# Kernel tuning notes

Hardware: AMD Instinct MI355X
Metric: run time of the kernel (lower is better)

The kernel has to match this reference:

```python
import jax, jax.numpy as jnp
import numpy as np

B, T, I, H, NM = 128, 512, 2, 1024, 8
MS = H // NM  # module size = 128


def setup_inputs() -> dict:
    key = jax.random.key(0)
    ks = jax.random.split(key, 6)
    s = 1.0 / np.sqrt(H)
    return {
        "x": jax.random.normal(ks[0], (B, T + 1, I, 1), jnp.float32),
        "W_ih": jax.random.normal(ks[1], (H, I), jnp.float32) * s,
        "W_hh": jax.random.normal(ks[2], (H, H), jnp.float32) * s,
        "fc_w": jax.random.normal(ks[3], (I, H), jnp.float32) * s,
        "fc_b": jax.random.normal(ks[4], (I,), jnp.float32) * s,
        "enc_w": jax.random.normal(ks[5], (H, I), jnp.float32) * s,
    }


def reference(x, W_ih, W_hh, fc_w, fc_b, enc_w):
    # x: [B, T+1, I, 1] -> squeeze trailing dim
    xs = x[..., 0]                       # [B, T+1, I]
    h0 = xs[:, 0] @ enc_w.T              # start_encoder (no bias) -> [B, H]

    # Clockwork block structure: row-module i reads hidden cols >= i*MS.
    mod_idx = jnp.arange(H) // MS
    mask_hh = (mod_idx[None, :] >= mod_idx[:, None]).astype(W_hh.dtype)
    Whh_m = W_hh * mask_hh               # block upper-triangular recurrent weights
    periods = 2 ** jnp.arange(NM)        # module clock periods [1,2,4,...,128]

    def step(h, inp):
        x_t, t = inp                     # x_t: [B, I], t: scalar step index
        cand = jnp.tanh(x_t @ W_ih.T + h @ Whh_m.T)          # [B, H]
        active = jnp.repeat((t % periods) == 0, MS)          # [H] unit-level clock mask
        h_new = jnp.where(active[None, :], cand, h)          # inactive modules keep state
        return h_new, h_new @ fc_w.T + fc_b                  # fc output per step

    _, outs = jax.lax.scan(step, h0, (jnp.swapaxes(xs[:, 1:], 0, 1), jnp.arange(T)))
    return jnp.swapaxes(outs, 0, 1)      # [B, T, I]
```

## Files before the change

kernel.cpp:

```cpp
#include <hip/hip_runtime.h>
#include <hip/hip_fp16.h>
#include <math.h>

#define Bsz 128
#define Tsz 512
#define Hsz 1024
#define MS  128
#define NT  512


__global__ __launch_bounds__(256)
void retile_whh(const float* __restrict__ W, __half* __restrict__ WBr) {
    const int p = blockIdx.x + 1;
    const int t = threadIdx.x;
    int c = 0;
    while ((c+1)*(c+2)/2 <= p) ++c;
    const int r = p - c*(c+1)/2;
    __half* wb = WBr + (size_t)(p-1) * MS * MS;
    for (int idx = t; idx < MS*MS; idx += 256) {
        const int row = idx >> 7, j = idx & (MS-1);
        wb[idx] = __float2half(W[(size_t)(r*MS+row)*Hsz + c*MS + j]);
    }
}

__device__ __forceinline__ float fast_tanh(float x) {
    const float e = __expf(2.0f * x);
    return 1.0f - 2.0f * __builtin_amdgcn_rcpf(e + 1.0f);
}

template <int CTRL>
__device__ __forceinline__ float dpp_get(float v) {
    union { float f; int i; } u, o;
    u.f = v;
    o.i = __builtin_amdgcn_update_dpp(0, u.i, CTRL, 0xf, 0xf, true);
    return o.f;
}

__device__ __forceinline__ void pk_fma(float2& acc, float2 a, float2 b) {
    asm("v_pk_fma_f32 %0, %1, %2, %0" : "+v"(acc) : "v"(a), "v"(b));
}

union H4 { short4 s4; __half2 h2[2]; };
union F4 { float4 v; float2 h[2]; };

__global__ __launch_bounds__(NT)
void cwrnn_kernel(const float* __restrict__ x,
                  const float* __restrict__ W_ih,
                  const float* __restrict__ fc_w,
                  const float* __restrict__ fc_b,
                  const float* __restrict__ enc_w,
                  const float* __restrict__ Whh,
                  const __half* __restrict__ WBr,
                  float* __restrict__ out)
{
    __shared__ float   Sp2s[36][MS];
    __shared__ float   h_s[Hsz];
    __shared__ float   H0[2][MS];
    __shared__ float2  x_s[Tsz+1];
    __shared__ float2  wih_s[Hsz];
    __shared__ float2  fcw_s[Hsz];
    __shared__ float2  OpM0[2][8];
    __shared__ float2  OpHi[16];
    __shared__ float2  OpHiN[16];

    const int tid   = threadIdx.x;
    const int lane  = tid & 63;
    const int wave  = tid >> 6;
    const int b     = blockIdx.x;
    const int row00 = tid >> 2;
    const int jc    = tid & 3;

    const float2* xb = (const float2*)(x + (size_t)b*(Tsz+1)*2);
    float* outb = out + (size_t)b*Tsz*2;

    for (int i = tid; i < Tsz+1; i += NT) x_s[i] = xb[i];
    for (int i = tid; i < Hsz; i += NT) wih_s[i] = ((const float2*)W_ih)[i];
    for (int i = tid; i < Hsz; i += NT) fcw_s[i] = make_float2(fc_w[i], fc_w[Hsz+i]);
    if (tid < 16) { OpHi[tid] = make_float2(0.f,0.f); OpHiN[tid] = make_float2(0.f,0.f); }
    const float fb0 = fc_b[0], fb1 = fc_b[1];

    F4 w00[8], w01[8], w11[8];
    #pragma unroll
    for (int u = 0; u < 8; ++u) {
        const int uu = (u + 2*jc) & 7;
        const int j  = jc*32 + uu*4;
        w00[u].v = *(const float4*)(Whh + (size_t)row00*Hsz + j);
        w01[u].v = *(const float4*)(Whh + (size_t)row00*Hsz + MS + j);
        w11[u].v = *(const float4*)(Whh + (size_t)(MS + row00)*Hsz + MS + j);
    }
    short4 w02[8];
    #pragma unroll
    for (int u = 0; u < 8; ++u) {
        const int uu = (u + 2*jc) & 7;
        w02[u] = *(const short4*)(WBr + (size_t)2*MS*MS + row00*MS + jc*32 + uu*4);
    }

    {
        const float2 x0 = xb[0];
        for (int i = tid; i < Hsz; i += NT) {
            const float2 ew = ((const float2*)enc_w)[i];
            const float v = x0.x*ew.x + x0.y*ew.y;
            h_s[i] = v;
            if (i < MS) H0[0][i] = v;
        }
    }
    __syncthreads();

    float R1=0.f,R2=0.f,R3=0.f,R4=0.f,R5=0.f,R6=0.f,R7=0.f;

    auto load_hq = [&](int c, F4* hq) {
        #pragma unroll
        for (int u = 0; u < 8; ++u) {
            const int uu = (u + 2*jc) & 7;
            hq[u].v = *(const float4*)(h_s + c*MS + jc*32 + uu*4);
        }
    };
    auto pair_acc32 = [&](const F4* w, const F4* hq) -> float {
        float2 a0 = {0.f,0.f}, a1 = {0.f,0.f};
        #pragma unroll
        for (int u = 0; u < 8; ++u) {
            pk_fma(a0, w[u].h[0], hq[u].h[0]);
            pk_fma(a1, w[u].h[1], hq[u].h[1]);
        }
        return (a0.x + a0.y) + (a1.x + a1.y);
    };
    auto pair_acc16 = [&](const short4* w, const F4* hq) -> float {
        float2 a0 = {0.f,0.f}, a1 = {0.f,0.f};
        #pragma unroll
        for (int u = 0; u < 8; ++u) {
            H4 ww; ww.s4 = w[u];
            pk_fma(a0, __half22float2(ww.h2[0]), hq[u].h[0]);
            pk_fma(a1, __half22float2(ww.h2[1]), hq[u].h[1]);
        }
        return (a0.x + a0.y) + (a1.x + a1.y);
    };
    auto wg_load = [&](int p, short4* w) {
        const __half* base = WBr + (size_t)(p-1)*MS*MS + row00*MS;
        #pragma unroll
        for (int u = 0; u < 8; ++u) {
            const int uu = (u + 2*jc) & 7;
            w[u] = *(const short4*)(base + jc*32 + uu*4);
        }
    };

    auto do_cols = [&](int ashad) {
        F4 hq[8];
        short4 wA[8], wB[8];
        if (ashad >= 2) wg_load(4, wA);
        load_hq(1, hq);
        R1 = pair_acc32(w01, hq);
        { float aa = pair_acc32(w11, hq);
          aa += dpp_get<0xB1>(aa); aa += dpp_get<0x4E>(aa);
          if (jc == 0) Sp2s[2][row00] = aa; }
        if (ashad >= 2) {
            load_hq(2, hq);
            R2 = pair_acc16(w02, hq);
            int cc = 2, rr = 1;
            while (true) {
                int rn = rr + 1, cn = cc;
                if (rn > cn) { cn += 1; rn = 0; }
                const bool hn = (cn <= ashad);
                if (hn) wg_load(cn*(cn+1)/2 + rn, wB);
                float aa = pair_acc16(wA, hq);
                if (rr == 0) {
                    switch (cc) {
                        case 3: R3 = aa; break;
                        case 4: R4 = aa; break;
                        case 5: R5 = aa; break;
                        case 6: R6 = aa; break;
                        default: R7 = aa; break;
                    }
                } else {
                    aa += dpp_get<0xB1>(aa); aa += dpp_get<0x4E>(aa);
                    if (jc == 0) Sp2s[cc*(cc+1)/2 + rr][row00] = aa;
                }
                if (!hn) break;
                if (cn != cc) load_hq(cn, hq);
                cc = cn; rr = rn;
                #pragma unroll
                for (int u = 0; u < 8; ++u) wA[u] = wB[u];
            }
        }
    };

    do_cols(7);
    __syncthreads();

    for (int t = 0; t < Tsz; ++t) {
        const int A  = (t == 0) ? 7 : ((t & 1) ? 0 : min(__ffs(t)-1, 7));
        const int ap = (t & 1) ? ((t == 1) ? 7 : min(__ffs(t-1)-1, 7)) : 0;
        const float2 xt = x_s[t+1];

        if (ap >= 1) do_cols(ap);

        {
            const float* h0r = H0[t & 1];
            float2 a0 = {0.f,0.f}, a1 = {0.f,0.f};
            #pragma unroll
            for (int u = 0; u < 8; ++u) {
                const int uu = (u + 2*jc) & 7;
                F4 hv; hv.v = *(const float4*)(h0r + jc*32 + uu*4);
                pk_fma(a0, w00[u].h[0], hv.h[0]);
                pk_fma(a1, w00[u].h[1], hv.h[1]);
            }
            float a = (a0.x + a0.y) + (a1.x + a1.y);
            a += ((R1+R2)+(R3+R4)) + ((R5+R6)+R7);
            a += dpp_get<0xB1>(a); a += dpp_get<0x4E>(a);
            const float2 wih0 = wih_s[row00];
            const float hv0 = fast_tanh(a + xt.x*wih0.x + xt.y*wih0.y);
            if (jc == 0) H0[(t+1)&1][row00] = hv0;
            const float2 fw0 = fcw_s[row00];
            float o0 = (jc == 0) ? hv0*fw0.x : 0.f;
            float o1 = (jc == 0) ? hv0*fw0.y : 0.f;
            o0 += dpp_get<0x111>(o0); o1 += dpp_get<0x111>(o1);
            o0 += dpp_get<0x112>(o0); o1 += dpp_get<0x112>(o1);
            o0 += dpp_get<0x114>(o0); o1 += dpp_get<0x114>(o1);
            o0 += dpp_get<0x118>(o0); o1 += dpp_get<0x118>(o1);
            o0 += dpp_get<0x142>(o0); o1 += dpp_get<0x142>(o1);
            o0 += dpp_get<0x143>(o0); o1 += dpp_get<0x143>(o1);
            if (lane == 63) OpM0[t&1][wave] = make_float2(o0, o1);
        }

        if (A >= 1) {
            const int nrows = (A+1)*MS;
            {
                const int g = MS + tid;
                if (g < nrows) {
                    const int r = g >> 7, il = g & (MS-1);
                    float sc[8];
                    #pragma unroll
                    for (int c = 1; c < 8; ++c)
                        sc[c] = Sp2s[c*(c+1)/2 + ((c < r) ? c : r)][il];
                    const float2 wih2 = wih_s[g];
                    float pre = xt.x*wih2.x + xt.y*wih2.y;
                    #pragma unroll
                    for (int c = 1; c < 8; ++c) pre += (c >= r) ? sc[c] : 0.f;
                    const float hv = fast_tanh(pre);
                    h_s[g] = hv;
                    const float2 fw = fcw_s[g];
                    float o0 = hv*fw.x, o1 = hv*fw.y;
                    o0 += dpp_get<0x111>(o0); o1 += dpp_get<0x111>(o1);
                    o0 += dpp_get<0x112>(o0); o1 += dpp_get<0x112>(o1);
                    o0 += dpp_get<0x114>(o0); o1 += dpp_get<0x114>(o1);
                    o0 += dpp_get<0x118>(o0); o1 += dpp_get<0x118>(o1);
                    o0 += dpp_get<0x142>(o0); o1 += dpp_get<0x142>(o1);
                    o0 += dpp_get<0x143>(o0); o1 += dpp_get<0x143>(o1);
                    if (lane == 63) OpHiN[2 + wave] = make_float2(o0, o1);
                }
            }
            {
                const int g = 5*MS + tid;
                if (g < nrows) {
                    const int r = g >> 7, il = g & (MS-1);
                    float sc[8];
                    #pragma unroll
                    for (int c = 1; c < 8; ++c)
                        sc[c] = Sp2s[c*(c+1)/2 + ((c < r) ? c : r)][il];
                    const float2 wih2 = wih_s[g];
                    float pre = xt.x*wih2.x + xt.y*wih2.y;
                    #pragma unroll
                    for (int c = 1; c < 8; ++c) pre += (c >= r) ? sc[c] : 0.f;
                    const float hv = fast_tanh(pre);
                    h_s[g] = hv;
                    const float2 fw = fcw_s[g];
                    float o0 = hv*fw.x, o1 = hv*fw.y;
                    o0 += dpp_get<0x111>(o0); o1 += dpp_get<0x111>(o1);
                    o0 += dpp_get<0x112>(o0); o1 += dpp_get<0x112>(o1);
                    o0 += dpp_get<0x114>(o0); o1 += dpp_get<0x114>(o1);
                    o0 += dpp_get<0x118>(o0); o1 += dpp_get<0x118>(o1);
                    o0 += dpp_get<0x142>(o0); o1 += dpp_get<0x142>(o1);
                    o0 += dpp_get<0x143>(o0); o1 += dpp_get<0x143>(o1);
                    if (lane == 63) OpHiN[10 + wave] = make_float2(o0, o1);
                }
            }
        }

        if (t > 0 && tid == 0) {
            const int tp = t - 1;
            if (ap >= 1) {
                for (int k = 2; k <= 2*ap+1; ++k) OpHi[k] = OpHiN[k];
            }
            float o0 = fb0, o1 = fb1;
            #pragma unroll
            for (int w = 0; w < 8; ++w) { o0 += OpM0[tp&1][w].x; o1 += OpM0[tp&1][w].y; }
            #pragma unroll
            for (int k = 2; k < 16; ++k) { o0 += OpHi[k].x; o1 += OpHi[k].y; }
            *(float2*)(outb + 2*tp) = make_float2(o0, o1);
        }

        __syncthreads();
    }

    if (tid == 0) {
        float o0 = fb0, o1 = fb1;
        #pragma unroll
        for (int w = 0; w < 8; ++w) { o0 += OpM0[1][w].x; o1 += OpM0[1][w].y; }
        #pragma unroll
        for (int k = 2; k < 16; ++k) { o0 += OpHi[k].x; o1 += OpHi[k].y; }
        *(float2*)(outb + 2*(Tsz-1)) = make_float2(o0, o1);
    }
}

extern "C" void kernel_launch(void* const* d_in, const int* in_sizes, int n_in,
                              void* d_out, int out_size, void* d_ws, size_t ws_size,
                              hipStream_t stream) {
    const float* x     = (const float*)d_in[0];
    const float* W_ih  = (const float*)d_in[1];
    const float* W_hh  = (const float*)d_in[2];
    const float* fc_w  = (const float*)d_in[3];
    const float* fc_b  = (const float*)d_in[4];
    const float* enc_w = (const float*)d_in[5];
    float* outp = (float*)d_out;
    __half* WBr = (__half*)((char*)d_ws + 65536);

    retile_whh<<<35, 256, 0, stream>>>(W_hh, WBr);
    cwrnn_kernel<<<Bsz, NT, 0, stream>>>(x, W_ih, fc_w, fc_b, enc_w, W_hh, WBr, outp);
}
```

Before: 1.087 ms.

## Hold more fp16 recurrent blocks in registers and prefetch module-0 hidden state

Converts the register-resident W01 and W11 blocks from fp32 to fp16 and adds W12 and W22 as register-resident fp16 blocks. The streamed-weight loop therefore starts at column 3 instead of column 2. Weight loads become 16-byte int4 loads without the per-thread rotation, and the module-0 hidden vector is loaded before do_cols so its latency overlaps that work. Adds launch_bounds minimum blocks of 2, which constrains registers and risks spills. Removing the rotation may also raise LDS bank conflicts, and fp16 for W01/W11 lowers precision.

```diff
diff --git a/kernel.cpp b/kernel.cpp
--- a/kernel.cpp
+++ b/kernel.cpp
@@ -43,7 +43,7 @@
 union H4 { short4 s4; __half2 h2[2]; };
 union F4 { float4 v; float2 h[2]; };
 
-__global__ __launch_bounds__(NT)
+__global__ __launch_bounds__(NT, 2)
 void cwrnn_kernel(const float* __restrict__ x,
                   const float* __restrict__ W_ih,
                   const float* __restrict__ fc_w,
@@ -79,20 +79,22 @@
     if (tid < 16) { OpHi[tid] = make_float2(0.f,0.f); OpHiN[tid] = make_float2(0.f,0.f); }
     const float fb0 = fc_b[0], fb1 = fc_b[1];
 
-    F4 w00[8], w01[8], w11[8];
+    F4 w00[8];
     #pragma unroll
-    for (int u = 0; u < 8; ++u) {
-        const int uu = (u + 2*jc) & 7;
-        const int j  = jc*32 + uu*4;
-        w00[u].v = *(const float4*)(Whh + (size_t)row00*Hsz + j);
-        w01[u].v = *(const float4*)(Whh + (size_t)row00*Hsz + MS + j);
-        w11[u].v = *(const float4*)(Whh + (size_t)(MS + row00)*Hsz + MS + j);
-    }
-    short4 w02[8];
-    #pragma unroll
-    for (int u = 0; u < 8; ++u) {
-        const int uu = (u + 2*jc) & 7;
-        w02[u] = *(const short4*)(WBr + (size_t)2*MS*MS + row00*MS + jc*32 + uu*4);
+    for (int u = 0; u < 8; ++u)
+        w00[u].v = *(const float4*)(Whh + (size_t)row00*Hsz + jc*32 + u*4);
+
+    short4 w01[8], w02[8], w11[8], w12[8], w22[8];
+    {
+        const __half* base = WBr + row00*MS + jc*32;
+        #pragma unroll
+        for (int u = 0; u < 4; ++u) {
+            *(int4*)(&w01[2*u]) = *(const int4*)(base + (size_t)0*MS*MS + u*8);
+            *(int4*)(&w11[2*u]) = *(const int4*)(base + (size_t)1*MS*MS + u*8);
+            *(int4*)(&w02[2*u]) = *(const int4*)(base + (size_t)2*MS*MS + u*8);
+            *(int4*)(&w12[2*u]) = *(const int4*)(base + (size_t)3*MS*MS + u*8);
+            *(int4*)(&w22[2*u]) = *(const int4*)(base + (size_t)4*MS*MS + u*8);
+        }
     }
 
     {
@@ -110,19 +112,8 @@
 
     auto load_hq = [&](int c, F4* hq) {
         #pragma unroll
-        for (int u = 0; u < 8; ++u) {
-            const int uu = (u + 2*jc) & 7;
-            hq[u].v = *(const float4*)(h_s + c*MS + jc*32 + uu*4);
-        }
-    };
-    auto pair_acc32 = [&](const F4* w, const F4* hq) -> float {
-        float2 a0 = {0.f,0.f}, a1 = {0.f,0.f};
-        #pragma unroll
-        for (int u = 0; u < 8; ++u) {
-            pk_fma(a0, w[u].h[0], hq[u].h[0]);
-            pk_fma(a1, w[u].h[1], hq[u].h[1]);
-        }
-        return (a0.x + a0.y) + (a1.x + a1.y);
+        for (int u = 0; u < 8; ++u)
+            hq[u].v = *(const float4*)(h_s + c*MS + jc*32 + u*4);
     };
     auto pair_acc16 = [&](const short4* w, const F4* hq) -> float {
         float2 a0 = {0.f,0.f}, a1 = {0.f,0.f};
@@ -135,27 +126,34 @@
         return (a0.x + a0.y) + (a1.x + a1.y);
     };
     auto wg_load = [&](int p, short4* w) {
-        const __half* base = WBr + (size_t)(p-1)*MS*MS + row00*MS;
-        #pragma unroll
-        for (int u = 0; u < 8; ++u) {
-            const int uu = (u + 2*jc) & 7;
-            w[u] = *(const short4*)(base + jc*32 + uu*4);
-        }
+        const __half* base = WBr + (size_t)(p-1)*MS*MS + row00*MS + jc*32;
+        #pragma unroll
+        for (int u = 0; u < 4; ++u)
+            *(int4*)(&w[2*u]) = *(const int4*)(base + u*8);
     };
 
     auto do_cols = [&](int ashad) {
         F4 hq[8];
         short4 wA[8], wB[8];
-        if (ashad >= 2) wg_load(4, wA);
+        if (ashad >= 3) wg_load(6, wA);
         load_hq(1, hq);
-        R1 = pair_acc32(w01, hq);
-        { float aa = pair_acc32(w11, hq);
+        R1 = pair_acc16(w01, hq);
+        { float aa = pair_acc16(w11, hq);
           aa += dpp_get<0xB1>(aa); aa += dpp_get<0x4E>(aa);
           if (jc == 0) Sp2s[2][row00] = aa; }
         if (ashad >= 2) {
             load_hq(2, hq);
             R2 = pair_acc16(w02, hq);
-            int cc = 2, rr = 1;
+            { float aa = pair_acc16(w12, hq);
+              aa += dpp_get<0xB1>(aa); aa += dpp_get<0x4E>(aa);
+              if (jc == 0) Sp2s[4][row00] = aa; }
+            { float aa = pair_acc16(w22, hq);
+              aa += dpp_get<0xB1>(aa); aa += dpp_get<0x4E>(aa);
+              if (jc == 0) Sp2s[5][row00] = aa; }
+        }
+        if (ashad >= 3) {
+            load_hq(3, hq);
+            int cc = 3, rr = 0;
             while (true) {
                 int rn = rr + 1, cn = cc;
                 if (rn > cn) { cn += 1; rn = 0; }
@@ -191,17 +189,22 @@
         const int ap = (t & 1) ? ((t == 1) ? 7 : min(__ffs(t-1)-1, 7)) : 0;
         const float2 xt = x_s[t+1];
 
-        if (ap >= 1) do_cols(ap);
-
+        F4 h0q[8];
         {
             const float* h0r = H0[t & 1];
+            #pragma unroll
+            for (int u = 0; u < 8; ++u)
+                h0q[u].v = *(const float4*)(h0r + jc*32 + u*4);
+        }
+
+        if (ap >= 1) do_cols(ap);
+
+        {
             float2 a0 = {0.f,0.f}, a1 = {0.f,0.f};
             #pragma unroll
             for (int u = 0; u < 8; ++u) {
-                const int uu = (u + 2*jc) & 7;
-                F4 hv; hv.v = *(const float4*)(h0r + jc*32 + uu*4);
-                pk_fma(a0, w00[u].h[0], hv.h[0]);
-                pk_fma(a1, w00[u].h[1], hv.h[1]);
+                pk_fma(a0, w00[u].h[0], h0q[u].h[0]);
+                pk_fma(a1, w00[u].h[1], h0q[u].h[1]);
             }
             float a = (a0.x + a0.y) + (a1.x + a1.y);
             a += ((R1+R2)+(R3+R4)) + ((R5+R6)+R7);
```

After: 1.341 ms. +23.4%, slower.

## Pre-swizzle fp16 weight tiles, drop fp32 register copies, parallelize output reduction

Applied to the files above, without the earlier changes.

The retile kernel now stores each fp16 W_hh block already permuted to match the per-thread rotated column order, so wg_load can fetch 16-byte vectors instead of eight scattered 8-byte loads. The fp32 register-resident blocks w01/w11 and fp16 w02 are removed, and those tiles are streamed from the fp16 workspace like the others. This lowers register pressure but adds global/L2 traffic per step and reduces precision for those blocks. The per-step output reduction moves from a serial single-thread loop to a wave-level shuffle reduction, with outputs buffered in LDS and written to global memory once at the end.

```diff
diff --git a/kernel.cpp b/kernel.cpp
--- a/kernel.cpp
+++ b/kernel.cpp
@@ -18,8 +18,10 @@
     const int r = p - c*(c+1)/2;
     __half* wb = WBr + (size_t)(p-1) * MS * MS;
     for (int idx = t; idx < MS*MS; idx += 256) {
-        const int row = idx >> 7, j = idx & (MS-1);
-        wb[idx] = __float2half(W[(size_t)(r*MS+row)*Hsz + c*MS + j]);
+        const int row = idx >> 7, rem = idx & 127;
+        const int jcq = rem >> 5, k = (rem >> 3) & 3, e = rem & 7;
+        const int src_col = jcq*32 + (((k + jcq) & 3) << 3) + e;
+        wb[idx] = __float2half(W[(size_t)(r*MS+row)*Hsz + c*MS + src_col]);
     }
 }
 
@@ -62,6 +64,7 @@
     __shared__ float2  OpM0[2][8];
     __shared__ float2  OpHi[16];
     __shared__ float2  OpHiN[16];
+    __shared__ float   out_s[Tsz*2];
 
     const int tid   = threadIdx.x;
     const int lane  = tid & 63;
@@ -79,20 +82,11 @@
     if (tid < 16) { OpHi[tid] = make_float2(0.f,0.f); OpHiN[tid] = make_float2(0.f,0.f); }
     const float fb0 = fc_b[0], fb1 = fc_b[1];
 
-    F4 w00[8], w01[8], w11[8];
+    F4 w00[8];
     #pragma unroll
     for (int u = 0; u < 8; ++u) {
         const int uu = (u + 2*jc) & 7;
-        const int j  = jc*32 + uu*4;
-        w00[u].v = *(const float4*)(Whh + (size_t)row00*Hsz + j);
-        w01[u].v = *(const float4*)(Whh + (size_t)row00*Hsz + MS + j);
-        w11[u].v = *(const float4*)(Whh + (size_t)(MS + row00)*Hsz + MS + j);
-    }
-    short4 w02[8];
-    #pragma unroll
-    for (int u = 0; u < 8; ++u) {
-        const int uu = (u + 2*jc) & 7;
-        w02[u] = *(const short4*)(WBr + (size_t)2*MS*MS + row00*MS + jc*32 + uu*4);
+        w00[u].v = *(const float4*)(Whh + (size_t)row00*Hsz + jc*32 + uu*4);
     }
 
     {
@@ -114,15 +108,6 @@
             const int uu = (u + 2*jc) & 7;
             hq[u].v = *(const float4*)(h_s + c*MS + jc*32 + uu*4);
         }
-    };
-    auto pair_acc32 = [&](const F4* w, const F4* hq) -> float {
-        float2 a0 = {0.f,0.f}, a1 = {0.f,0.f};
-        #pragma unroll
-        for (int u = 0; u < 8; ++u) {
-            pk_fma(a0, w[u].h[0], hq[u].h[0]);
-            pk_fma(a1, w[u].h[1], hq[u].h[1]);
-        }
-        return (a0.x + a0.y) + (a1.x + a1.y);
     };
     auto pair_acc16 = [&](const short4* w, const F4* hq) -> float {
         float2 a0 = {0.f,0.f}, a1 = {0.f,0.f};
@@ -135,27 +120,26 @@
         return (a0.x + a0.y) + (a1.x + a1.y);
     };
     auto wg_load = [&](int p, short4* w) {
-        const __half* base = WBr + (size_t)(p-1)*MS*MS + row00*MS;
+        const __half* base = WBr + (size_t)(p-1)*MS*MS + row00*MS + jc*32;
         #pragma unroll
-        for (int u = 0; u < 8; ++u) {
-            const int uu = (u + 2*jc) & 7;
-            w[u] = *(const short4*)(base + jc*32 + uu*4);
-        }
+        for (int k = 0; k < 4; ++k)
+            *(int4*)(&w[2*k]) = *(const int4*)(base + k*8);
     };
 
     auto do_cols = [&](int ashad) {
+        short4 wA[8], wB[8];
         F4 hq[8];
-        short4 wA[8], wB[8];
-        if (ashad >= 2) wg_load(4, wA);
+        wg_load(1, wA);
+        wg_load(2, wB);
         load_hq(1, hq);
-        R1 = pair_acc32(w01, hq);
-        { float aa = pair_acc32(w11, hq);
+        R1 = pair_acc16(wA, hq);
+        { float aa = pair_acc16(wB, hq);
           aa += dpp_get<0xB1>(aa); aa += dpp_get<0x4E>(aa);
           if (jc == 0) Sp2s[2][row00] = aa; }
         if (ashad >= 2) {
+            wg_load(3, wA);
             load_hq(2, hq);
-            R2 = pair_acc16(w02, hq);
-            int cc = 2, rr = 1;
+            int cc = 2, rr = 0;
             while (true) {
                 int rn = rr + 1, cn = cc;
                 if (rn > cn) { cn += 1; rn = 0; }
@@ -164,6 +148,7 @@
                 float aa = pair_acc16(wA, hq);
                 if (rr == 0) {
                     switch (cc) {
+                        case 2: R2 = aa; break;
                         case 3: R3 = aa; break;
                         case 4: R4 = aa; break;
                         case 5: R5 = aa; break;
@@ -275,30 +260,46 @@
             }
         }
 
-        if (t > 0 && tid == 0) {
+        if (t > 0 && wave == 0) {
             const int tp = t - 1;
-            if (ap >= 1) {
-                for (int k = 2; k <= 2*ap+1; ++k) OpHi[k] = OpHiN[k];
-            }
-            float o0 = fb0, o1 = fb1;
+            if (ap >= 1 && lane >= 2 && lane <= 2*ap + 1)
+                OpHi[lane] = OpHiN[lane];
+            asm volatile("s_waitcnt lgkmcnt(0)" ::: "memory");
+            float2 v = make_float2(0.f, 0.f);
+            if (lane < 8)                  v = OpM0[tp & 1][lane];
+            else if (lane < 22)            v = OpHi[lane - 6];
+            float o0 = v.x, o1 = v.y;
             #pragma unroll
-            for (int w = 0; w < 8; ++w) { o0 += OpM0[tp&1][w].x; o1 += OpM0[tp&1][w].y; }
-            #pragma unroll
-            for (int k = 2; k < 16; ++k) { o0 += OpHi[k].x; o1 += OpHi[k].y; }
-            *(float2*)(outb + 2*tp) = make_float2(o0, o1);
+            for (int off = 1; off < 64; off <<= 1) {
+                o0 += __shfl_xor(o0, off, 64);
+                o1 += __shfl_xor(o1, off, 64);
+            }
+            if (lane == 0) {
+                out_s[2*tp]   = o0 + fb0;
+                out_s[2*tp+1] = o1 + fb1;
+            }
         }
 
         __syncthreads();
     }
 
-    if (tid == 0) {
-        float o0 = fb0, o1 = fb1;
+    if (wave == 0) {
+        float2 v = make_float2(0.f, 0.f);
+        if (lane < 8)       v = OpM0[1][lane];
+        else if (lane < 22) v = OpHi[lane - 6];
+        float o0 = v.x, o1 = v.y;
         #pragma unroll
-        for (int w = 0; w < 8; ++w) { o0 += OpM0[1][w].x; o1 += OpM0[1][w].y; }
-        #pragma unroll
-        for (int k = 2; k < 16; ++k) { o0 += OpHi[k].x; o1 += OpHi[k].y; }
-        *(float2*)(outb + 2*(Tsz-1)) = make_float2(o0, o1);
-    }
+        for (int off = 1; off < 64; off <<= 1) {
+            o0 += __shfl_xor(o0, off, 64);
+            o1 += __shfl_xor(o1, off, 64);
+        }
+        if (lane == 0) {
+            out_s[2*(Tsz-1)]   = o0 + fb0;
+            out_s[2*(Tsz-1)+1] = o1 + fb1;
+        }
+    }
+    __syncthreads();
+    for (int i = tid; i < Tsz*2; i += NT) outb[i] = out_s[i];
 }
 
 extern "C" void kernel_launch(void* const* d_in, const int* in_sizes, int n_in,
```

Result: slower. 1.291 ms (+18.8%).
